# Kernel optimization log

Hardware: AMD Instinct MI355X
Metric: run time of the kernel (lower is better)

## Reference

```python
import jax, jax.numpy as jnp
import numpy as np

N_NODES = 100000
N_EDGES = 1600000
IN_F, HID_F, OUT_F = 64, 64, 16


def setup_inputs() -> dict:
    key = jax.random.key(0)
    k_x, k_e, k_w1, k_w2 = jax.random.split(key, 4)
    x = jax.random.normal(k_x, (N_NODES, IN_F), dtype=jnp.float32)
    edge_index = jax.random.randint(k_e, (2, N_EDGES), 0, N_NODES, dtype=jnp.int64)
    # Glorot-ish init for the GCNConv linear weights; bias zeros (PyG default)
    W1 = jax.random.normal(k_w1, (IN_F, HID_F), dtype=jnp.float32) / np.sqrt(IN_F)
    b1 = jnp.zeros((HID_F,), dtype=jnp.float32)
    W2 = jax.random.normal(k_w2, (HID_F, OUT_F), dtype=jnp.float32) / np.sqrt(HID_F)
    b2 = jnp.zeros((OUT_F,), dtype=jnp.float32)
    return {"x": x, "edge_index": edge_index, "W1": W1, "b1": b1, "W2": W2, "b2": b2}


def reference(x, edge_index, W1, b1, W2, b2):
    N = x.shape[0]
    # GCNConv: add self-loops, symmetric normalization D^-1/2 A D^-1/2
    loop = jnp.arange(N, dtype=edge_index.dtype)
    src = jnp.concatenate([edge_index[0], loop])  # [E+N]
    dst = jnp.concatenate([edge_index[1], loop])  # [E+N]
    deg = jax.ops.segment_sum(jnp.ones_like(dst, dtype=x.dtype), dst, num_segments=N)
    dis = jax.lax.rsqrt(deg)  # deg >= 1 due to self-loops
    norm = dis[src] * dis[dst]  # [E+N]

    def gcn_conv(h, W, b):
        h = h @ W                                   # [N, d_out]
        msg = h[src] * norm[:, None]                # gather + scale  [E+N, d_out]
        agg = jax.ops.segment_sum(msg, dst, num_segments=N)  # scatter-add
        return agg + b

    h = jax.nn.relu(gcn_conv(x, W1, b1))
    h = gcn_conv(h, W2, b2)
    return jax.nn.log_softmax(h, axis=1)
```

## Files before the change

### kernel.cpp

```cpp
#include <hip/hip_runtime.h>
#include <hip/hip_bf16.h>
#include <hip/hip_fp16.h>


#define F1 64
#define F2 16
#define NBKT 256
#define BSH 512
#define NSB 256
#define SBD 1024
#define STG 9216

typedef _Float16 f16x8 __attribute__((ext_vector_type(8)));
typedef _Float16 f16x4 __attribute__((ext_vector_type(4)));
typedef _Float16 f16x2 __attribute__((ext_vector_type(2)));
typedef float f32x4 __attribute__((ext_vector_type(4)));

__device__ inline f16x8 shfl_xor_f16x8(f16x8 v, int off) {
  union U { f16x8 h; int i[4]; } a, b;
  a.h = v;
#pragma unroll
  for (int k = 0; k < 4; ++k) b.i[k] = __shfl_xor(a.i[k], off);
  return b.h;
}
__device__ inline f16x4 shfl_xor_f16x4(f16x4 v, int off) {
  union U { f16x4 h; int i[2]; } a, b;
  a.h = v;
#pragma unroll
  for (int k = 0; k < 2; ++k) b.i[k] = __shfl_xor(a.i[k], off);
  return b.h;
}

__global__ void k_scatterL(const int* __restrict__ src, const int* __restrict__ dst,
                           int* __restrict__ tmp, int* __restrict__ segstart,
                           int E, int nb, int chunk,
                           const float* __restrict__ W1, const float* __restrict__ W2,
                           __half* __restrict__ W1T, __half* __restrict__ W2T) {
  int t = threadIdx.x, sb = blockIdx.x;
  if (sb == NSB) {
    for (int i = t; i < 64 * 64; i += SBD) {
      int n = i >> 6, k = i & 63;
      W1T[i] = __float2half(W1[k * 64 + n]);
    }
    for (int i = t; i < 16 * 64; i += SBD) {
      int n = i >> 6, k = i & 63;
      W2T[i] = __float2half(W2[k * 16 + n]);
    }
    return;
  }
  __shared__ int h[NBKT];
  __shared__ int cur[NBKT];
  __shared__ int sc[NBKT];
  int beg = sb * chunk, end = min(beg + chunk, E);
  for (int i = t; i < NBKT; i += SBD) h[i] = 0;
  __syncthreads();
  int e;
  for (e = beg + t * 4; e + 4 <= end; e += 4 * SBD) {
    int4 d4 = *(const int4*)(dst + e);
    atomicAdd(&h[d4.x >> 9], 1);
    atomicAdd(&h[d4.y >> 9], 1);
    atomicAdd(&h[d4.z >> 9], 1);
    atomicAdd(&h[d4.w >> 9], 1);
  }
  for (; e < end; ++e) atomicAdd(&h[dst[e] >> 9], 1);
  __syncthreads();
  if (t < NBKT) sc[t] = h[t];
  __syncthreads();
  for (int off = 1; off < NBKT; off <<= 1) {
    int a = (t < NBKT && t >= off) ? sc[t - off] : 0;
    __syncthreads();
    if (t < NBKT) sc[t] += a;
    __syncthreads();
  }
  if (t < NBKT) cur[t] = (t == 0) ? 0 : sc[t - 1];
  __syncthreads();
  for (int i = t; i < nb; i += SBD) segstart[sb * (nb + 1) + i] = beg + cur[i];
  if (t == 0) segstart[sb * (nb + 1) + nb] = end;
  __syncthreads();
  for (e = beg + t * 4; e + 4 <= end; e += 4 * SBD) {
    int4 d4 = *(const int4*)(dst + e);
    int4 s4 = *(const int4*)(src + e);
    int b, off;
    b = d4.x >> 9; off = atomicAdd(&cur[b], 1); tmp[beg + off] = (s4.x << 9) | (d4.x & 511);
    b = d4.y >> 9; off = atomicAdd(&cur[b], 1); tmp[beg + off] = (s4.y << 9) | (d4.y & 511);
    b = d4.z >> 9; off = atomicAdd(&cur[b], 1); tmp[beg + off] = (s4.z << 9) | (d4.z & 511);
    b = d4.w >> 9; off = atomicAdd(&cur[b], 1); tmp[beg + off] = (s4.w << 9) | (d4.w & 511);
  }
  for (; e < end; ++e) {
    int d = dst[e];
    int b = d >> 9;
    int off = atomicAdd(&cur[b], 1);
    tmp[beg + off] = (src[e] << 9) | (d & 511);
  }
}

__global__ void k_csr(const int* __restrict__ tmp, const int* __restrict__ segstart,
                      int* __restrict__ csr, int* __restrict__ rowptr,
                      float* __restrict__ dis, int N, int nb, int chunk) {
  __shared__ int stage[STG];
  __shared__ int sc[BSH];
  __shared__ int cnt[BSH];
  __shared__ int lofs[BSH];
  __shared__ int s_beg;
  int b = blockIdx.x, t = threadIdx.x;
  int s0 = 0, len = 0;
  if (t < NSB) {
    s0 = segstart[t * (nb + 1) + b];
    len = segstart[t * (nb + 1) + b + 1] - s0;
  }
  sc[t] = (t < NSB) ? (s0 - t * chunk) : 0;
  __syncthreads();
  for (int off = BSH / 2; off > 0; off >>= 1) {
    if (t < off) sc[t] += sc[t + off];
    __syncthreads();
  }
  if (t == 0) s_beg = sc[0];
  __syncthreads();
  int beg = s_beg;
  sc[t] = (t < NSB) ? len : 0;
  __syncthreads();
  for (int off = 1; off < NSB; off <<= 1) {
    int a = (t < NSB && t >= off) ? sc[t - off] : 0;
    __syncthreads();
    if (t < NSB) sc[t] += a;
    __syncthreads();
  }
  int total = sc[NSB - 1];
  int my0 = (t == 0) ? 0 : ((t < NSB) ? sc[t - 1] : 0);
  if (t < NSB) {
    int i = 0;
    for (; i + 4 <= len; i += 4) {
      int v0 = tmp[s0 + i], v1 = tmp[s0 + i + 1], v2 = tmp[s0 + i + 2], v3 = tmp[s0 + i + 3];
      stage[my0 + i] = v0; stage[my0 + i + 1] = v1;
      stage[my0 + i + 2] = v2; stage[my0 + i + 3] = v3;
    }
    for (; i < len; ++i) stage[my0 + i] = tmp[s0 + i];
  }
  cnt[t] = 0;
  __syncthreads();
  for (int i = t; i < total; i += BSH) atomicAdd(&cnt[stage[i] & (BSH - 1)], 1);
  __syncthreads();
  sc[t] = cnt[t];
  __syncthreads();
  for (int off = 1; off < BSH; off <<= 1) {
    int a = (t >= off) ? sc[t - off] : 0;
    __syncthreads();
    sc[t] += a;
    __syncthreads();
  }
  int excl = (t == 0) ? 0 : sc[t - 1];
  lofs[t] = excl;
  int n = b * BSH + t;
  if (n <= N) rowptr[n] = beg + excl;
  if (n < N) dis[n] = rsqrtf((float)(cnt[t] + 1));
  cnt[t] = 0;
  __syncthreads();
  for (int i = t; i < total; i += BSH) {
    int p = stage[i];
    int l = p & (BSH - 1);
    int off = atomicAdd(&cnt[l], 1);
    csr[beg + lofs[l] + off] = p >> 9;
  }
}

__global__ void k_gemm1(const float* __restrict__ x, const __half* __restrict__ W1T,
                        const float* __restrict__ dis, __half* __restrict__ out, int N) {
  int t = threadIdx.x;
  int wv = t >> 6, lane = t & 63;
  int m = lane & 15, q = lane >> 4;
  int row0 = blockIdx.x * 64 + wv * 16;
  int arow = min(row0 + m, N - 1);
  const _Float16* wt = (const _Float16*)W1T;
  f16x8 bf[4][2];
#pragma unroll
  for (int c = 0; c < 4; ++c)
#pragma unroll
    for (int kt = 0; kt < 2; ++kt)
      bf[c][kt] = *(const f16x8*)&wt[(c * 16 + m) * 64 + kt * 32 + q * 8];
  f16x8 a[2];
#pragma unroll
  for (int kt = 0; kt < 2; ++kt) {
    const float4* xp = (const float4*)(x + (size_t)arow * 64 + kt * 32 + q * 8);
    float4 u = xp[0], v = xp[1];
    a[kt][0] = (_Float16)u.x; a[kt][1] = (_Float16)u.y;
    a[kt][2] = (_Float16)u.z; a[kt][3] = (_Float16)u.w;
    a[kt][4] = (_Float16)v.x; a[kt][5] = (_Float16)v.y;
    a[kt][6] = (_Float16)v.z; a[kt][7] = (_Float16)v.w;
  }
  f32x4 acc[4] = {};
#pragma unroll
  for (int kt = 0; kt < 2; ++kt)
#pragma unroll
    for (int c = 0; c < 4; ++c)
      acc[c] = __builtin_amdgcn_mfma_f32_16x16x32_f16(a[kt], bf[c][kt], acc[c], 0, 0, 0);
#pragma unroll
  for (int r = 0; r < 4; ++r) {
    int n = row0 + q * 4 + r;
    if (n < N) {
      float dn = dis[n];
#pragma unroll
      for (int c = 0; c < 4; ++c)
        out[(size_t)n * 64 + c * 16 + m] = __float2half(acc[c][r] * dn);
    }
  }
}

__global__ void k_agg1f(const __half* __restrict__ h, const float* __restrict__ dis,
                        const int* __restrict__ rowptr, const int* __restrict__ csr,
                        const float* __restrict__ b1, const __half* __restrict__ W2T,
                        __half* __restrict__ h2, int N) {
  int gt = blockIdx.x * blockDim.x + threadIdx.x;
  int w = gt >> 6;
  int lane = gt & 63;
  int half = lane >> 5;
  int sub = (lane >> 3) & 3;
  int fl = lane & 7;
  int n = w * 2 + half;
  if (n >= N) return;
  const _Float16* hp = (const _Float16*)h;
  float dn = dis[n];
  float4 bu = *(const float4*)(b1 + fl * 8);
  float4 bv = *(const float4*)(b1 + fl * 8 + 4);
  const _Float16* wt = (const _Float16*)W2T;
  f16x8 wj[4];
#pragma unroll
  for (int i = 0; i < 4; ++i)
    wj[i] = *(const f16x8*)&wt[(sub * 4 + i) * 64 + fl * 8];
  f16x8 acc0 = {}, acc1 = {};
  if (sub == 0)
    acc0 = *(const f16x8*)&hp[(size_t)n * 64 + fl * 8];
  int beg = rowptr[n], end = rowptr[n + 1];
  int e = beg + sub;
  int sA = (e < end) ? csr[e] : -1;
  int sB = (e + 4 < end) ? csr[e + 4] : -1;
  while (sB >= 0) {
    int e2 = e + 8;
    int sC = (e2 < end) ? csr[e2] : -1;
    int sD = (e2 + 4 < end) ? csr[e2 + 4] : -1;
    f16x8 v0 = *(const f16x8*)&hp[(size_t)sA * 64 + fl * 8];
    f16x8 v1 = *(const f16x8*)&hp[(size_t)sB * 64 + fl * 8];
    acc0 += v0;
    acc1 += v1;
    sA = sC; sB = sD; e = e2;
  }
  if (sA >= 0)
    acc0 += *(const f16x8*)&hp[(size_t)sA * 64 + fl * 8];
  f16x8 acc = acc0 + acc1;
  acc += shfl_xor_f16x8(acc, 8);
  acc += shfl_xor_f16x8(acc, 16);
  float bb[8] = {bu.x, bu.y, bu.z, bu.w, bv.x, bv.y, bv.z, bv.w};
  f16x8 hr16;
#pragma unroll
  for (int k = 0; k < 8; ++k)
    hr16[k] = (_Float16)fmaxf(fmaf(dn, (float)acc[k], bb[k]), 0.f);
  const f16x2* h2v = (const f16x2*)&hr16;
  float p[4];
#pragma unroll
  for (int i = 0; i < 4; ++i) {
    const f16x2* wv = (const f16x2*)&wj[i];
    f16x2 qq = {};
#pragma unroll
    for (int k = 0; k < 4; ++k) qq += h2v[k] * wv[k];
    float pi = (float)qq[0] + (float)qq[1];
    pi += __shfl_xor(pi, 1);
    pi += __shfl_xor(pi, 2);
    pi += __shfl_xor(pi, 4);
    p[i] = pi;
  }
  if (fl == 0) {
    f16x4 o;
#pragma unroll
    for (int i = 0; i < 4; ++i) o[i] = (_Float16)(p[i] * dn);
    *(f16x4*)((_Float16*)h2 + (size_t)n * 16 + sub * 4) = o;
  }
}

__global__ void k_agg2(const __half* __restrict__ h2, const float* __restrict__ dis,
                       const int* __restrict__ rowptr, const int* __restrict__ csr,
                       const float* __restrict__ b2, float* __restrict__ out, int N) {
  int gt = blockIdx.x * blockDim.x + threadIdx.x;
  int w = gt >> 6;
  int lane = gt & 63;
  int half = lane >> 5;
  int sub = (lane >> 2) & 7;
  int fl = lane & 3;
  int n = w * 2 + half;
  if (n >= N) return;
  const _Float16* hp = (const _Float16*)h2;
  f16x4 acc0 = {}, acc1 = {};
  if (sub == 0)
    acc0 = *(const f16x4*)&hp[(size_t)n * 16 + fl * 4];
  int beg = rowptr[n], end = rowptr[n + 1];
  int e = beg + sub;
  int sA = (e < end) ? csr[e] : -1;
  int sB = (e + 8 < end) ? csr[e + 8] : -1;
  while (sB >= 0) {
    int e2 = e + 16;
    int sC = (e2 < end) ? csr[e2] : -1;
    int sD = (e2 + 8 < end) ? csr[e2 + 8] : -1;
    f16x4 v0 = *(const f16x4*)&hp[(size_t)sA * 16 + fl * 4];
    f16x4 v1 = *(const f16x4*)&hp[(size_t)sB * 16 + fl * 4];
    acc0 += v0;
    acc1 += v1;
    sA = sC; sB = sD; e = e2;
  }
  if (sA >= 0)
    acc0 += *(const f16x4*)&hp[(size_t)sA * 16 + fl * 4];
  f16x4 acc = acc0 + acc1;
  acc += shfl_xor_f16x4(acc, 4);
  acc += shfl_xor_f16x4(acc, 8);
  acc += shfl_xor_f16x4(acc, 16);
  if (sub == 0) {
    float dn = dis[n];
    float4 bb = *(const float4*)(b2 + fl * 4);
    float v0 = fmaf(dn, (float)acc[0], bb.x);
    float v1 = fmaf(dn, (float)acc[1], bb.y);
    float v2 = fmaf(dn, (float)acc[2], bb.z);
    float v3 = fmaf(dn, (float)acc[3], bb.w);
    float m = fmaxf(fmaxf(v0, v1), fmaxf(v2, v3));
    m = fmaxf(m, __shfl_xor(m, 1));
    m = fmaxf(m, __shfl_xor(m, 2));
    float s2 = __expf(v0 - m) + __expf(v1 - m) + __expf(v2 - m) + __expf(v3 - m);
    s2 += __shfl_xor(s2, 1);
    s2 += __shfl_xor(s2, 2);
    float ls = m + __logf(s2);
    float4 o = {v0 - ls, v1 - ls, v2 - ls, v3 - ls};
    *(float4*)(out + (size_t)n * 16 + fl * 4) = o;
  }
}

extern "C" void kernel_launch(void* const* d_in, const int* in_sizes, int n_in,
                              void* d_out, int out_size, void* d_ws, size_t ws_size,
                              hipStream_t stream) {
  const float* x = (const float*)d_in[0];
  const int* ei = (const int*)d_in[1];
  const float* W1 = (const float*)d_in[2];
  const float* b1 = (const float*)d_in[3];
  const float* W2 = (const float*)d_in[4];
  const float* b2 = (const float*)d_in[5];
  float* out = (float*)d_out;

  int N = in_sizes[0] / F1;
  int E = in_sizes[1] / 2;
  const int* src = ei;
  const int* dst = ei + E;
  int nb = (N + BSH - 1) >> 9;
  int chunk = ((E + NSB - 1) / NSB + 3) & ~3;

  char* ws = (char*)d_ws;
  size_t o_w1t   = 0;
  size_t o_w2t   = o_w1t + 64 * 64 * 2;
  size_t o_seg   = (o_w2t + 16 * 64 * 2 + 255) & ~(size_t)255;
  size_t o_dis   = (o_seg + (size_t)NSB * (nb + 1) * 4 + 255) & ~(size_t)255;
  size_t o_rowp  = (o_dis + (size_t)N * 4 + 255) & ~(size_t)255;
  size_t o_tmp   = (o_rowp + (size_t)(N + 1) * 4 + 255) & ~(size_t)255;
  size_t o_csr   = (o_tmp + (size_t)NSB * chunk * 4 + 255) & ~(size_t)255;
  size_t o_h1    = (o_csr + (size_t)E * 4 + 255) & ~(size_t)255;
  size_t o_h2    = (o_h1 + (size_t)N * 64 * 2 + 255) & ~(size_t)255;

  __half* W1T  = (__half*)(ws + o_w1t);
  __half* W2T  = (__half*)(ws + o_w2t);
  int* segst   = (int*)(ws + o_seg);
  float* dis   = (float*)(ws + o_dis);
  int* rowptr  = (int*)(ws + o_rowp);
  int* tmp     = (int*)(ws + o_tmp);
  int* csr     = (int*)(ws + o_csr);
  __half* h1   = (__half*)(ws + o_h1);
  __half* h2   = (__half*)(ws + o_h2);

  k_scatterL<<<NSB + 1, SBD, 0, stream>>>(src, dst, tmp, segst, E, nb, chunk,
                                          W1, W2, W1T, W2T);
  k_csr<<<nb, BSH, 0, stream>>>(tmp, segst, csr, rowptr, dis, N, nb, chunk);

  int gb = (N + 63) / 64;
  k_gemm1<<<gb, 256, 0, stream>>>(x, W1T, dis, h1, N);
  int aw = (N + 1) / 2;
  k_agg1f<<<((size_t)aw * 64 + 255) / 256, 256, 0, stream>>>(h1, dis, rowptr, csr, b1, W2T, h2, N);
  k_agg2<<<((size_t)aw * 64 + 255) / 256, 256, 0, stream>>>(h2, dis, rowptr, csr, b2, out, N);
}
```

Before: 174.0 us.

## Fuse all five GCN stages into one cooperative persistent kernel with grid syncs

```diff
diff --git a/kernel.cpp b/kernel.cpp
--- a/kernel.cpp
+++ b/kernel.cpp
@@ -1,6 +1,9 @@
 #include <hip/hip_runtime.h>
 #include <hip/hip_bf16.h>
 #include <hip/hip_fp16.h>
+#include <hip/hip_cooperative_groups.h>
+
+namespace cg = cooperative_groups;
 
 
 #define F1 64
@@ -8,7 +11,8 @@
 #define NBKT 256
 #define BSH 512
 #define NSB 256
-#define SBD 1024
+#define NBLK 256
+#define BDIM 1024
 #define STG 9216
 
 typedef _Float16 f16x8 __attribute__((ext_vector_type(8)));
@@ -31,301 +35,306 @@
   return b.h;
 }
 
-__global__ void k_scatterL(const int* __restrict__ src, const int* __restrict__ dst,
-                           int* __restrict__ tmp, int* __restrict__ segstart,
-                           int E, int nb, int chunk,
-                           const float* __restrict__ W1, const float* __restrict__ W2,
-                           __half* __restrict__ W1T, __half* __restrict__ W2T) {
+__global__ void __launch_bounds__(BDIM, 1) k_fused(
+    const int* __restrict__ src, const int* __restrict__ dst,
+    const float* __restrict__ x, const float* __restrict__ W1,
+    const float* __restrict__ b1, const float* __restrict__ W2,
+    const float* __restrict__ b2, int* __restrict__ tmp,
+    int* __restrict__ segstart, int* __restrict__ csr,
+    int* __restrict__ rowptr, float* __restrict__ dis,
+    __half* __restrict__ W1T, __half* __restrict__ W2T,
+    __half* __restrict__ h1, __half* __restrict__ h2,
+    float* __restrict__ out, int N, int E, int nb, int chunk) {
+  cg::grid_group grid = cg::this_grid();
+  __shared__ int sA[BSH];
+  __shared__ int sB[BSH];
+  __shared__ int sC[BSH];
+  __shared__ int sStage[STG];
   int t = threadIdx.x, sb = blockIdx.x;
-  if (sb == NSB) {
-    for (int i = t; i < 64 * 64; i += SBD) {
+
+  if (sb == 0) {
+    for (int i = t; i < 64 * 64; i += BDIM) {
       int n = i >> 6, k = i & 63;
       W1T[i] = __float2half(W1[k * 64 + n]);
     }
-    for (int i = t; i < 16 * 64; i += SBD) {
+    for (int i = t; i < 16 * 64; i += BDIM) {
       int n = i >> 6, k = i & 63;
       W2T[i] = __float2half(W2[k * 16 + n]);
     }
-    return;
-  }
-  __shared__ int h[NBKT];
-  __shared__ int cur[NBKT];
-  __shared__ int sc[NBKT];
-  int beg = sb * chunk, end = min(beg + chunk, E);
-  for (int i = t; i < NBKT; i += SBD) h[i] = 0;
-  __syncthreads();
-  int e;
-  for (e = beg + t * 4; e + 4 <= end; e += 4 * SBD) {
-    int4 d4 = *(const int4*)(dst + e);
-    atomicAdd(&h[d4.x >> 9], 1);
-    atomicAdd(&h[d4.y >> 9], 1);
-    atomicAdd(&h[d4.z >> 9], 1);
-    atomicAdd(&h[d4.w >> 9], 1);
-  }
-  for (; e < end; ++e) atomicAdd(&h[dst[e] >> 9], 1);
-  __syncthreads();
-  if (t < NBKT) sc[t] = h[t];
-  __syncthreads();
-  for (int off = 1; off < NBKT; off <<= 1) {
-    int a = (t < NBKT && t >= off) ? sc[t - off] : 0;
-    __syncthreads();
-    if (t < NBKT) sc[t] += a;
-    __syncthreads();
-  }
-  if (t < NBKT) cur[t] = (t == 0) ? 0 : sc[t - 1];
-  __syncthreads();
-  for (int i = t; i < nb; i += SBD) segstart[sb * (nb + 1) + i] = beg + cur[i];
-  if (t == 0) segstart[sb * (nb + 1) + nb] = end;
-  __syncthreads();
-  for (e = beg + t * 4; e + 4 <= end; e += 4 * SBD) {
-    int4 d4 = *(const int4*)(dst + e);
-    int4 s4 = *(const int4*)(src + e);
-    int b, off;
-    b = d4.x >> 9; off = atomicAdd(&cur[b], 1); tmp[beg + off] = (s4.x << 9) | (d4.x & 511);
-    b = d4.y >> 9; off = atomicAdd(&cur[b], 1); tmp[beg + off] = (s4.y << 9) | (d4.y & 511);
-    b = d4.z >> 9; off = atomicAdd(&cur[b], 1); tmp[beg + off] = (s4.z << 9) | (d4.z & 511);
-    b = d4.w >> 9; off = atomicAdd(&cur[b], 1); tmp[beg + off] = (s4.w << 9) | (d4.w & 511);
-  }
-  for (; e < end; ++e) {
-    int d = dst[e];
-    int b = d >> 9;
-    int off = atomicAdd(&cur[b], 1);
-    tmp[beg + off] = (src[e] << 9) | (d & 511);
-  }
-}
-
-__global__ void k_csr(const int* __restrict__ tmp, const int* __restrict__ segstart,
-                      int* __restrict__ csr, int* __restrict__ rowptr,
-                      float* __restrict__ dis, int N, int nb, int chunk) {
-  __shared__ int stage[STG];
-  __shared__ int sc[BSH];
-  __shared__ int cnt[BSH];
-  __shared__ int lofs[BSH];
-  __shared__ int s_beg;
-  int b = blockIdx.x, t = threadIdx.x;
-  int s0 = 0, len = 0;
-  if (t < NSB) {
-    s0 = segstart[t * (nb + 1) + b];
-    len = segstart[t * (nb + 1) + b + 1] - s0;
-  }
-  sc[t] = (t < NSB) ? (s0 - t * chunk) : 0;
-  __syncthreads();
-  for (int off = BSH / 2; off > 0; off >>= 1) {
-    if (t < off) sc[t] += sc[t + off];
-    __syncthreads();
-  }
-  if (t == 0) s_beg = sc[0];
-  __syncthreads();
-  int beg = s_beg;
-  sc[t] = (t < NSB) ? len : 0;
-  __syncthreads();
-  for (int off = 1; off < NSB; off <<= 1) {
-    int a = (t < NSB && t >= off) ? sc[t - off] : 0;
-    __syncthreads();
-    if (t < NSB) sc[t] += a;
-    __syncthreads();
-  }
-  int total = sc[NSB - 1];
-  int my0 = (t == 0) ? 0 : ((t < NSB) ? sc[t - 1] : 0);
-  if (t < NSB) {
-    int i = 0;
-    for (; i + 4 <= len; i += 4) {
-      int v0 = tmp[s0 + i], v1 = tmp[s0 + i + 1], v2 = tmp[s0 + i + 2], v3 = tmp[s0 + i + 3];
-      stage[my0 + i] = v0; stage[my0 + i + 1] = v1;
-      stage[my0 + i + 2] = v2; stage[my0 + i + 3] = v3;
-    }
-    for (; i < len; ++i) stage[my0 + i] = tmp[s0 + i];
-  }
-  cnt[t] = 0;
-  __syncthreads();
-  for (int i = t; i < total; i += BSH) atomicAdd(&cnt[stage[i] & (BSH - 1)], 1);
-  __syncthreads();
-  sc[t] = cnt[t];
-  __syncthreads();
-  for (int off = 1; off < BSH; off <<= 1) {
-    int a = (t >= off) ? sc[t - off] : 0;
-    __syncthreads();
-    sc[t] += a;
-    __syncthreads();
-  }
-  int excl = (t == 0) ? 0 : sc[t - 1];
-  lofs[t] = excl;
-  int n = b * BSH + t;
-  if (n <= N) rowptr[n] = beg + excl;
-  if (n < N) dis[n] = rsqrtf((float)(cnt[t] + 1));
-  cnt[t] = 0;
-  __syncthreads();
-  for (int i = t; i < total; i += BSH) {
-    int p = stage[i];
-    int l = p & (BSH - 1);
-    int off = atomicAdd(&cnt[l], 1);
-    csr[beg + lofs[l] + off] = p >> 9;
-  }
-}
-
-__global__ void k_gemm1(const float* __restrict__ x, const __half* __restrict__ W1T,
-                        const float* __restrict__ dis, __half* __restrict__ out, int N) {
-  int t = threadIdx.x;
-  int wv = t >> 6, lane = t & 63;
-  int m = lane & 15, q = lane >> 4;
-  int row0 = blockIdx.x * 64 + wv * 16;
-  int arow = min(row0 + m, N - 1);
-  const _Float16* wt = (const _Float16*)W1T;
-  f16x8 bf[4][2];
-#pragma unroll
-  for (int c = 0; c < 4; ++c)
-#pragma unroll
-    for (int kt = 0; kt < 2; ++kt)
-      bf[c][kt] = *(const f16x8*)&wt[(c * 16 + m) * 64 + kt * 32 + q * 8];
-  f16x8 a[2];
-#pragma unroll
-  for (int kt = 0; kt < 2; ++kt) {
-    const float4* xp = (const float4*)(x + (size_t)arow * 64 + kt * 32 + q * 8);
-    float4 u = xp[0], v = xp[1];
-    a[kt][0] = (_Float16)u.x; a[kt][1] = (_Float16)u.y;
-    a[kt][2] = (_Float16)u.z; a[kt][3] = (_Float16)u.w;
-    a[kt][4] = (_Float16)v.x; a[kt][5] = (_Float16)v.y;
-    a[kt][6] = (_Float16)v.z; a[kt][7] = (_Float16)v.w;
-  }
-  f32x4 acc[4] = {};
-#pragma unroll
-  for (int kt = 0; kt < 2; ++kt)
+  }
+  {
+    int beg = sb * chunk, end = min(beg + chunk, E);
+    for (int i = t; i < NBKT; i += BDIM) sA[i] = 0;
+    __syncthreads();
+    int e;
+    for (e = beg + t * 4; e + 4 <= end; e += 4 * BDIM) {
+      int4 d4 = *(const int4*)(dst + e);
+      atomicAdd(&sA[d4.x >> 9], 1);
+      atomicAdd(&sA[d4.y >> 9], 1);
+      atomicAdd(&sA[d4.z >> 9], 1);
+      atomicAdd(&sA[d4.w >> 9], 1);
+    }
+    for (; e < end; ++e) atomicAdd(&sA[dst[e] >> 9], 1);
+    __syncthreads();
+    if (t < NBKT) sB[t] = sA[t];
+    __syncthreads();
+    for (int off = 1; off < NBKT; off <<= 1) {
+      int a = (t < NBKT && t >= off) ? sB[t - off] : 0;
+      __syncthreads();
+      if (t < NBKT) sB[t] += a;
+      __syncthreads();
+    }
+    if (t < NBKT) sC[t] = (t == 0) ? 0 : sB[t - 1];
+    __syncthreads();
+    for (int i = t; i < nb; i += BDIM) segstart[sb * (nb + 1) + i] = beg + sC[i];
+    if (t == 0) segstart[sb * (nb + 1) + nb] = end;
+    __syncthreads();
+    for (e = beg + t * 4; e + 4 <= end; e += 4 * BDIM) {
+      int4 d4 = *(const int4*)(dst + e);
+      int4 s4 = *(const int4*)(src + e);
+      int b, off;
+      b = d4.x >> 9; off = atomicAdd(&sC[b], 1); tmp[beg + off] = (s4.x << 9) | (d4.x & 511);
+      b = d4.y >> 9; off = atomicAdd(&sC[b], 1); tmp[beg + off] = (s4.y << 9) | (d4.y & 511);
+      b = d4.z >> 9; off = atomicAdd(&sC[b], 1); tmp[beg + off] = (s4.z << 9) | (d4.z & 511);
+      b = d4.w >> 9; off = atomicAdd(&sC[b], 1); tmp[beg + off] = (s4.w << 9) | (d4.w & 511);
+    }
+    for (; e < end; ++e) {
+      int d = dst[e];
+      int b = d >> 9;
+      int off = atomicAdd(&sC[b], 1);
+      tmp[beg + off] = (src[e] << 9) | (d & 511);
+    }
+  }
+  grid.sync();
+
+  if (sb < nb) {
+    int b = sb;
+    int s0 = 0, len = 0;
+    if (t < NSB) {
+      s0 = segstart[t * (nb + 1) + b];
+      len = segstart[t * (nb + 1) + b + 1] - s0;
+    }
+    if (t < NSB) sA[t] = s0 - t * chunk;
+    __syncthreads();
+    for (int off = NSB / 2; off > 0; off >>= 1) {
+      if (t < off) sA[t] += sA[t + off];
+      __syncthreads();
+    }
+    int beg = sA[0];
+    __syncthreads();
+    if (t < NSB) { sB[t] = len; sC[t] = s0; }
+    __syncthreads();
+    for (int off = 1; off < NSB; off <<= 1) {
+      int a = (t < NSB && t >= off) ? sB[t - off] : 0;
+      __syncthreads();
+      if (t < NSB) sB[t] += a;
+      __syncthreads();
+    }
+    int total = sB[NSB - 1];
+    {
+      int seg = t >> 2, l4 = t & 3;
+      int sbeg = (seg == 0) ? 0 : sB[seg - 1];
+      int slen = sB[seg] - sbeg;
+      int ssrc = sC[seg];
+      for (int i = l4; i < slen; i += 4) sStage[sbeg + i] = tmp[ssrc + i];
+    }
+    __syncthreads();
+    if (t < BSH) sA[t] = 0;
+    __syncthreads();
+    for (int i = t; i < total; i += BDIM) atomicAdd(&sA[sStage[i] & (BSH - 1)], 1);
+    __syncthreads();
+    if (t < BSH) sB[t] = sA[t];
+    __syncthreads();
+    for (int off = 1; off < BSH; off <<= 1) {
+      int a = (t < BSH && t >= off) ? sB[t - off] : 0;
+      __syncthreads();
+      if (t < BSH) sB[t] += a;
+      __syncthreads();
+    }
+    if (t < BSH) {
+      int excl = (t == 0) ? 0 : sB[t - 1];
+      sC[t] = excl;
+      int n = b * BSH + t;
+      if (n <= N) rowptr[n] = beg + excl;
+      if (n < N) dis[n] = rsqrtf((float)(sA[t] + 1));
+    }
+    __syncthreads();
+    if (t < BSH) sA[t] = 0;
+    __syncthreads();
+    for (int i = t; i < total; i += BDIM) {
+      int p = sStage[i];
+      int l = p & (BSH - 1);
+      int off = atomicAdd(&sA[l], 1);
+      csr[beg + sC[l] + off] = p >> 9;
+    }
+  }
+  grid.sync();
+
+  {
+    int wv = t >> 6, lane = t & 63;
+    int m = lane & 15, q = lane >> 4;
+    const _Float16* wt = (const _Float16*)W1T;
+    f16x8 bf[4][2];
 #pragma unroll
     for (int c = 0; c < 4; ++c)
-      acc[c] = __builtin_amdgcn_mfma_f32_16x16x32_f16(a[kt], bf[c][kt], acc[c], 0, 0, 0);
-#pragma unroll
-  for (int r = 0; r < 4; ++r) {
-    int n = row0 + q * 4 + r;
-    if (n < N) {
-      float dn = dis[n];
-#pragma unroll
-      for (int c = 0; c < 4; ++c)
-        out[(size_t)n * 64 + c * 16 + m] = __float2half(acc[c][r] * dn);
-    }
-  }
-}
-
-__global__ void k_agg1f(const __half* __restrict__ h, const float* __restrict__ dis,
-                        const int* __restrict__ rowptr, const int* __restrict__ csr,
-                        const float* __restrict__ b1, const __half* __restrict__ W2T,
-                        __half* __restrict__ h2, int N) {
-  int gt = blockIdx.x * blockDim.x + threadIdx.x;
-  int w = gt >> 6;
-  int lane = gt & 63;
-  int half = lane >> 5;
-  int sub = (lane >> 3) & 3;
-  int fl = lane & 7;
-  int n = w * 2 + half;
-  if (n >= N) return;
-  const _Float16* hp = (const _Float16*)h;
-  float dn = dis[n];
-  float4 bu = *(const float4*)(b1 + fl * 8);
-  float4 bv = *(const float4*)(b1 + fl * 8 + 4);
-  const _Float16* wt = (const _Float16*)W2T;
-  f16x8 wj[4];
-#pragma unroll
-  for (int i = 0; i < 4; ++i)
-    wj[i] = *(const f16x8*)&wt[(sub * 4 + i) * 64 + fl * 8];
-  f16x8 acc0 = {}, acc1 = {};
-  if (sub == 0)
-    acc0 = *(const f16x8*)&hp[(size_t)n * 64 + fl * 8];
-  int beg = rowptr[n], end = rowptr[n + 1];
-  int e = beg + sub;
-  int sA = (e < end) ? csr[e] : -1;
-  int sB = (e + 4 < end) ? csr[e + 4] : -1;
-  while (sB >= 0) {
-    int e2 = e + 8;
-    int sC = (e2 < end) ? csr[e2] : -1;
-    int sD = (e2 + 4 < end) ? csr[e2 + 4] : -1;
-    f16x8 v0 = *(const f16x8*)&hp[(size_t)sA * 64 + fl * 8];
-    f16x8 v1 = *(const f16x8*)&hp[(size_t)sB * 64 + fl * 8];
-    acc0 += v0;
-    acc1 += v1;
-    sA = sC; sB = sD; e = e2;
-  }
-  if (sA >= 0)
-    acc0 += *(const f16x8*)&hp[(size_t)sA * 64 + fl * 8];
-  f16x8 acc = acc0 + acc1;
-  acc += shfl_xor_f16x8(acc, 8);
-  acc += shfl_xor_f16x8(acc, 16);
-  float bb[8] = {bu.x, bu.y, bu.z, bu.w, bv.x, bv.y, bv.z, bv.w};
-  f16x8 hr16;
-#pragma unroll
-  for (int k = 0; k < 8; ++k)
-    hr16[k] = (_Float16)fmaxf(fmaf(dn, (float)acc[k], bb[k]), 0.f);
-  const f16x2* h2v = (const f16x2*)&hr16;
-  float p[4];
-#pragma unroll
-  for (int i = 0; i < 4; ++i) {
-    const f16x2* wv = (const f16x2*)&wj[i];
-    f16x2 qq = {};
-#pragma unroll
-    for (int k = 0; k < 4; ++k) qq += h2v[k] * wv[k];
-    float pi = (float)qq[0] + (float)qq[1];
-    pi += __shfl_xor(pi, 1);
-    pi += __shfl_xor(pi, 2);
-    pi += __shfl_xor(pi, 4);
-    p[i] = pi;
-  }
-  if (fl == 0) {
-    f16x4 o;
-#pragma unroll
-    for (int i = 0; i < 4; ++i) o[i] = (_Float16)(p[i] * dn);
-    *(f16x4*)((_Float16*)h2 + (size_t)n * 16 + sub * 4) = o;
-  }
-}
-
-__global__ void k_agg2(const __half* __restrict__ h2, const float* __restrict__ dis,
-                       const int* __restrict__ rowptr, const int* __restrict__ csr,
-                       const float* __restrict__ b2, float* __restrict__ out, int N) {
-  int gt = blockIdx.x * blockDim.x + threadIdx.x;
-  int w = gt >> 6;
-  int lane = gt & 63;
-  int half = lane >> 5;
-  int sub = (lane >> 2) & 7;
-  int fl = lane & 3;
-  int n = w * 2 + half;
-  if (n >= N) return;
-  const _Float16* hp = (const _Float16*)h2;
-  f16x4 acc0 = {}, acc1 = {};
-  if (sub == 0)
-    acc0 = *(const f16x4*)&hp[(size_t)n * 16 + fl * 4];
-  int beg = rowptr[n], end = rowptr[n + 1];
-  int e = beg + sub;
-  int sA = (e < end) ? csr[e] : -1;
-  int sB = (e + 8 < end) ? csr[e + 8] : -1;
-  while (sB >= 0) {
-    int e2 = e + 16;
-    int sC = (e2 < end) ? csr[e2] : -1;
-    int sD = (e2 + 8 < end) ? csr[e2 + 8] : -1;
-    f16x4 v0 = *(const f16x4*)&hp[(size_t)sA * 16 + fl * 4];
-    f16x4 v1 = *(const f16x4*)&hp[(size_t)sB * 16 + fl * 4];
-    acc0 += v0;
-    acc1 += v1;
-    sA = sC; sB = sD; e = e2;
-  }
-  if (sA >= 0)
-    acc0 += *(const f16x4*)&hp[(size_t)sA * 16 + fl * 4];
-  f16x4 acc = acc0 + acc1;
-  acc += shfl_xor_f16x4(acc, 4);
-  acc += shfl_xor_f16x4(acc, 8);
-  acc += shfl_xor_f16x4(acc, 16);
-  if (sub == 0) {
-    float dn = dis[n];
-    float4 bb = *(const float4*)(b2 + fl * 4);
-    float v0 = fmaf(dn, (float)acc[0], bb.x);
-    float v1 = fmaf(dn, (float)acc[1], bb.y);
-    float v2 = fmaf(dn, (float)acc[2], bb.z);
-    float v3 = fmaf(dn, (float)acc[3], bb.w);
-    float m = fmaxf(fmaxf(v0, v1), fmaxf(v2, v3));
-    m = fmaxf(m, __shfl_xor(m, 1));
-    m = fmaxf(m, __shfl_xor(m, 2));
-    float s2 = __expf(v0 - m) + __expf(v1 - m) + __expf(v2 - m) + __expf(v3 - m);
-    s2 += __shfl_xor(s2, 1);
-    s2 += __shfl_xor(s2, 2);
-    float ls = m + __logf(s2);
-    float4 o = {v0 - ls, v1 - ls, v2 - ls, v3 - ls};
-    *(float4*)(out + (size_t)n * 16 + fl * 4) = o;
+#pragma unroll
+      for (int kt = 0; kt < 2; ++kt)
+        bf[c][kt] = *(const f16x8*)&wt[(c * 16 + m) * 64 + kt * 32 + q * 8];
+    for (int base = sb * 256; base < N; base += NBLK * 256) {
+      int row0 = base + wv * 16;
+      int arow = min(row0 + m, N - 1);
+      f16x8 a[2];
+#pragma unroll
+      for (int kt = 0; kt < 2; ++kt) {
+        const float4* xp = (const float4*)(x + (size_t)arow * 64 + kt * 32 + q * 8);
+        float4 u = xp[0], v = xp[1];
+        a[kt][0] = (_Float16)u.x; a[kt][1] = (_Float16)u.y;
+        a[kt][2] = (_Float16)u.z; a[kt][3] = (_Float16)u.w;
+        a[kt][4] = (_Float16)v.x; a[kt][5] = (_Float16)v.y;
+        a[kt][6] = (_Float16)v.z; a[kt][7] = (_Float16)v.w;
+      }
+      f32x4 acc[4] = {};
+#pragma unroll
+      for (int kt = 0; kt < 2; ++kt)
+#pragma unroll
+        for (int c = 0; c < 4; ++c)
+          acc[c] = __builtin_amdgcn_mfma_f32_16x16x32_f16(a[kt], bf[c][kt], acc[c], 0, 0, 0);
+#pragma unroll
+      for (int r = 0; r < 4; ++r) {
+        int n = row0 + q * 4 + r;
+        if (n < N) {
+          float dn = dis[n];
+#pragma unroll
+          for (int c = 0; c < 4; ++c)
+            h1[(size_t)n * 64 + c * 16 + m] = __float2half(acc[c][r] * dn);
+        }
+      }
+    }
+  }
+  grid.sync();
+
+  {
+    int wv = t >> 6, lane = t & 63;
+    int half = lane >> 5;
+    int sub = (lane >> 3) & 3;
+    int fl = lane & 7;
+    const _Float16* hp = (const _Float16*)h1;
+    const _Float16* wt = (const _Float16*)W2T;
+    float4 bu = *(const float4*)(b1 + fl * 8);
+    float4 bv = *(const float4*)(b1 + fl * 8 + 4);
+    f16x8 wj[4];
+#pragma unroll
+    for (int i = 0; i < 4; ++i)
+      wj[i] = *(const f16x8*)&wt[(sub * 4 + i) * 64 + fl * 8];
+    int gw = sb * 16 + wv;
+    for (int w = gw; w * 2 < N; w += NBLK * 16) {
+      int n = w * 2 + half;
+      if (n < N) {
+        float dn = dis[n];
+        f16x8 acc0 = {}, acc1 = {};
+        if (sub == 0)
+          acc0 = *(const f16x8*)&hp[(size_t)n * 64 + fl * 8];
+        int beg = rowptr[n], end = rowptr[n + 1];
+        int e = beg + sub;
+        int sA2 = (e < end) ? csr[e] : -1;
+        int sB2 = (e + 4 < end) ? csr[e + 4] : -1;
+        while (sB2 >= 0) {
+          int e2 = e + 8;
+          int sC2 = (e2 < end) ? csr[e2] : -1;
+          int sD2 = (e2 + 4 < end) ? csr[e2 + 4] : -1;
+          f16x8 v0 = *(const f16x8*)&hp[(size_t)sA2 * 64 + fl * 8];
+          f16x8 v1 = *(const f16x8*)&hp[(size_t)sB2 * 64 + fl * 8];
+          acc0 += v0;
+          acc1 += v1;
+          sA2 = sC2; sB2 = sD2; e = e2;
+        }
+        if (sA2 >= 0)
+          acc0 += *(const f16x8*)&hp[(size_t)sA2 * 64 + fl * 8];
+        f16x8 acc = acc0 + acc1;
+        acc += shfl_xor_f16x8(acc, 8);
+        acc += shfl_xor_f16x8(acc, 16);
+        float bb[8] = {bu.x, bu.y, bu.z, bu.w, bv.x, bv.y, bv.z, bv.w};
+        f16x8 hr16;
+#pragma unroll
+        for (int k = 0; k < 8; ++k)
+          hr16[k] = (_Float16)fmaxf(fmaf(dn, (float)acc[k], bb[k]), 0.f);
+        const f16x2* h2v = (const f16x2*)&hr16;
+        float p[4];
+#pragma unroll
+        for (int i = 0; i < 4; ++i) {
+          const f16x2* wv2 = (const f16x2*)&wj[i];
+          f16x2 qq = {};
+#pragma unroll
+          for (int k = 0; k < 4; ++k) qq += h2v[k] * wv2[k];
+          float pi = (float)qq[0] + (float)qq[1];
+          pi += __shfl_xor(pi, 1);
+          pi += __shfl_xor(pi, 2);
+          pi += __shfl_xor(pi, 4);
+          p[i] = pi;
+        }
+        if (fl == 0) {
+          f16x4 o;
+#pragma unroll
+          for (int i = 0; i < 4; ++i) o[i] = (_Float16)(p[i] * dn);
+          *(f16x4*)((_Float16*)h2 + (size_t)n * 16 + sub * 4) = o;
+        }
+      }
+    }
+  }
+  grid.sync();
+
+  {
+    int wv = t >> 6, lane = t & 63;
+    int half = lane >> 5;
+    int sub = (lane >> 2) & 7;
+    int fl = lane & 3;
+    const _Float16* hp = (const _Float16*)h2;
+    int gw = sb * 16 + wv;
+    for (int w = gw; w * 2 < N; w += NBLK * 16) {
+      int n = w * 2 + half;
+      if (n < N) {
+        f16x4 acc0 = {}, acc1 = {};
+        if (sub == 0)
+          acc0 = *(const f16x4*)&hp[(size_t)n * 16 + fl * 4];
+        int beg = rowptr[n], end = rowptr[n + 1];
+        int e = beg + sub;
+        int sA2 = (e < end) ? csr[e] : -1;
+        int sB2 = (e + 8 < end) ? csr[e + 8] : -1;
+        while (sB2 >= 0) {
+          int e2 = e + 16;
+          int sC2 = (e2 < end) ? csr[e2] : -1;
+          int sD2 = (e2 + 8 < end) ? csr[e2 + 8] : -1;
+          f16x4 v0 = *(const f16x4*)&hp[(size_t)sA2 * 16 + fl * 4];
+          f16x4 v1 = *(const f16x4*)&hp[(size_t)sB2 * 16 + fl * 4];
+          acc0 += v0;
+          acc1 += v1;
+          sA2 = sC2; sB2 = sD2; e = e2;
+        }
+        if (sA2 >= 0)
+          acc0 += *(const f16x4*)&hp[(size_t)sA2 * 16 + fl * 4];
+        f16x4 acc = acc0 + acc1;
+        acc += shfl_xor_f16x4(acc, 4);
+        acc += shfl_xor_f16x4(acc, 8);
+        acc += shfl_xor_f16x4(acc, 16);
+        if (sub == 0) {
+          float dn = dis[n];
+          float4 bb = *(const float4*)(b2 + fl * 4);
+          float v0 = fmaf(dn, (float)acc[0], bb.x);
+          float v1 = fmaf(dn, (float)acc[1], bb.y);
+          float v2 = fmaf(dn, (float)acc[2], bb.z);
+          float v3 = fmaf(dn, (float)acc[3], bb.w);
+          float m = fmaxf(fmaxf(v0, v1), fmaxf(v2, v3));
+          m = fmaxf(m, __shfl_xor(m, 1));
+          m = fmaxf(m, __shfl_xor(m, 2));
+          float s2 = __expf(v0 - m) + __expf(v1 - m) + __expf(v2 - m) + __expf(v3 - m);
+          s2 += __shfl_xor(s2, 1);
+          s2 += __shfl_xor(s2, 2);
+          float ls = m + __logf(s2);
+          float4 o = {v0 - ls, v1 - ls, v2 - ls, v3 - ls};
+          *(float4*)(out + (size_t)n * 16 + fl * 4) = o;
+        }
+      }
+    }
   }
 }
 
@@ -368,13 +377,7 @@
   __half* h1   = (__half*)(ws + o_h1);
   __half* h2   = (__half*)(ws + o_h2);
 
-  k_scatterL<<<NSB + 1, SBD, 0, stream>>>(src, dst, tmp, segst, E, nb, chunk,
-                                          W1, W2, W1T, W2T);
-  k_csr<<<nb, BSH, 0, stream>>>(tmp, segst, csr, rowptr, dis, N, nb, chunk);
-
-  int gb = (N + 63) / 64;
-  k_gemm1<<<gb, 256, 0, stream>>>(x, W1T, dis, h1, N);
-  int aw = (N + 1) / 2;
-  k_agg1f<<<((size_t)aw * 64 + 255) / 256, 256, 0, stream>>>(h1, dis, rowptr, csr, b1, W2T, h2, N);
-  k_agg2<<<((size_t)aw * 64 + 255) / 256, 256, 0, stream>>>(h2, dis, rowptr, csr, b2, out, N);
+  void* args[] = {&src, &dst, &x, &W1, &b1, &W2, &b2, &tmp, &segst, &csr,
+                  &rowptr, &dis, &W1T, &W2T, &h1, &h2, &out, &N, &E, &nb, &chunk};
+  hipLaunchCooperativeKernel((void*)k_fused, dim3(NBLK), dim3(BDIM), args, 0, stream);
 }
```

Measured after the change: 335.0 us. +92.5%, slower.
